# Kernel optimization log

Hardware: AMD Instinct MI355X
Metric: run time of the kernel (lower is better)

Reference implementation:

```python
import jax, jax.numpy as jnp
import numpy as np

NB_TF = 4          # brightness, contrast, invert-blend, gain
MAGS_PER_TF = 9    # magnitudes 0.1 .. 0.9 (range(1, int(mag*10)) with mag=1)
NB_OP = NB_TF * MAGS_PER_TF


def setup_inputs() -> dict:
    key = jax.random.key(0)
    k1, k2, k3 = jax.random.split(key, 3)
    B, C, H, W = 256, 3, 224, 224
    x = jax.random.uniform(k1, (B, C, H, W), dtype=jnp.float32)
    # per-image sampled op index (Categorical over a uniform distribution)
    sample = jax.random.randint(k2, (B,), 0, NB_OP)
    # per-op Bernoulli(prob=0.5) coin: 1 -> apply the op, 0 -> identity
    apply_mask = jax.random.randint(k3, (NB_OP,), 0, 2).astype(jnp.int32)
    return {"x": x, "sample": sample, "apply_mask": apply_mask}


def _apply_ops(x, sample, apply_mask):
    # Decode op index -> (tf type, magnitude). op_list layout: for tf in TFs:
    #   for m in 1..9: (tf, prob, m/10)
    tf_idx = sample // MAGS_PER_TF                       # [B]
    mag = ((sample % MAGS_PER_TF) + 1).astype(x.dtype) / 10.0
    mag = mag[:, None, None, None]                       # [B,1,1,1]

    mean = jnp.mean(x, axis=(1, 2, 3), keepdims=True)    # per-image mean
    t_bright = jnp.clip(x + mag, 0.0, 1.0)               # brightness shift
    t_contr = jnp.clip(mean + (x - mean) * (1.0 + mag), 0.0, 1.0)
    t_inv = (1.0 - mag) * x + mag * (1.0 - x)            # blend with inverted
    t_gain = jnp.clip(x * (1.0 + mag), 0.0, 1.0)         # multiplicative gain

    stack = jnp.stack([t_bright, t_contr, t_inv, t_gain], axis=1)  # [B,4,C,H,W]
    sel = tf_idx[:, None, None, None, None]              # [B,1,1,1,1]
    transformed = jnp.take_along_axis(stack, sel, axis=1)[:, 0]    # [B,C,H,W]

    applied = (apply_mask[sample] > 0)[:, None, None, None]
    return jnp.where(applied, transformed, x)


def reference(x, sample, apply_mask):
    # N_seqTF = 1 -> single round of sample -> gather -> transform -> scatter,
    # here expressed as a fully vectorized per-image select.
    return _apply_ops(x, sample, apply_mask)
```

## Files before the change

kernel.cpp:

```cpp
#include <hip/hip_runtime.h>

#define N_IMG   256
#define HW      (224 * 224)
#define CHW     (3 * HW)
#define V4      (CHW / 4)
#define THREADS 256

#define PARTS       7
#define PART_V4     (V4 / PARTS)
#define PER_THREAD  (PART_V4 / THREADS)

#define CHUNKS  (V4 / THREADS)

#define MAGS_PER_TF 9

__device__ __forceinline__ float clip01(float v) {
    return fminf(fmaxf(v, 0.0f), 1.0f);
}

__global__ __launch_bounds__(THREADS) void mean_kernel(
        const float* __restrict__ x,
        const int* __restrict__ sample,
        const int* __restrict__ apply_mask,
        float* __restrict__ partials ) {
    const int img  = blockIdx.y;
    const int part = blockIdx.x;
    const int s    = sample[img];
    const int tf   = s / MAGS_PER_TF;
    if (tf != 1 || apply_mask[s] <= 0) return;

    const float4* xp = (const float4*)x + (size_t)img * V4 + (size_t)part * PART_V4;
    float sum = 0.0f;
#pragma unroll
    for (int k = 0; k < PER_THREAD; ++k) {
        float4 v = xp[threadIdx.x + k * THREADS];
        sum += (v.x + v.y) + (v.z + v.w);
    }
#pragma unroll
    for (int off = 32; off > 0; off >>= 1)
        sum += __shfl_down(sum, off, 64);

    __shared__ float wsum[THREADS / 64];
    if ((threadIdx.x & 63) == 0) wsum[threadIdx.x >> 6] = sum;
    __syncthreads();
    if (threadIdx.x == 0) {
        float t = (wsum[0] + wsum[1]) + (wsum[2] + wsum[3]);
        partials[img * PARTS + part] = t;
    }
}

__global__ __launch_bounds__(THREADS) void apply_kernel(
        const float* __restrict__ x,
        const int* __restrict__ sample,
        const int* __restrict__ apply_mask,
        const float* __restrict__ partials,
        float* __restrict__ out) {
    const int img   = blockIdx.y;
    const int chunk = blockIdx.x;
    const int s     = sample[img];
    const int tf    = s / MAGS_PER_TF;
    const float mag = (float)(s % MAGS_PER_TF + 1) / 10.0f;
    const bool applied = apply_mask[s] > 0;

    const size_t idx = (size_t)img * V4 + (size_t)chunk * THREADS + threadIdx.x;
    const float4* xp = (const float4*)x;
    float4*       op = (float4*)out;

    float4 v = xp[idx];
    float4 r;

    if (!applied) {
        r = v;
    } else if (tf == 0) {
        r.x = clip01(v.x + mag);
        r.y = clip01(v.y + mag);
        r.z = clip01(v.z + mag);
        r.w = clip01(v.w + mag);
    } else if (tf == 1) {
        float mean = 0.0f;
#pragma unroll
        for (int p = 0; p < PARTS; ++p) mean += partials[img * PARTS + p];
        mean /= (float)CHW;
        const float g = 1.0f + mag;
        r.x = clip01(mean + (v.x - mean) * g);
        r.y = clip01(mean + (v.y - mean) * g);
        r.z = clip01(mean + (v.z - mean) * g);
        r.w = clip01(mean + (v.w - mean) * g);
    } else if (tf == 2) {
        const float a = 1.0f - mag;
        r.x = a * v.x + mag * (1.0f - v.x);
        r.y = a * v.y + mag * (1.0f - v.y);
        r.z = a * v.z + mag * (1.0f - v.z);
        r.w = a * v.w + mag * (1.0f - v.w);
    } else {
        const float g = 1.0f + mag;
        r.x = clip01(v.x * g);
        r.y = clip01(v.y * g);
        r.z = clip01(v.z * g);
        r.w = clip01(v.w * g);
    }
    op[idx] = r;
}

extern "C" void kernel_launch(void* const* d_in, const int* in_sizes, int n_in,
                              void* d_out, int out_size, void* d_ws, size_t ws_size,
                              hipStream_t stream) {
    const float* x          = (const float*)d_in[0];
    const int*   sample     = (const int*)d_in[1];
    const int*   apply_mask = (const int*)d_in[2];
    float*       out        = (float*)d_out;
    float*       partials   = (float*)d_ws;

    dim3 mgrid(PARTS, N_IMG);
    mean_kernel<<<mgrid, THREADS, 0, stream>>>(x, sample, apply_mask, partials);

    dim3 agrid(CHUNKS, N_IMG);
    apply_kernel<<<agrid, THREADS, 0, stream>>>(x, sample, apply_mask, partials, out);
}
```

Before: 262.1 us.

## Coarsen apply kernel to 7 float4 per thread with nontemporal stores

The apply kernel drops from one float4 per thread across 147 blocks per image to 7 float4 per thread across 21 blocks per image. All loads are issued before compute, and outputs are written with nontemporal stores. The mean kernel uses the same 21-chunk split and loads its values into registers first. The aim is to cut per-block overhead, raise memory-level parallelism, and keep the output stream out of cache. The cost is fewer blocks overall and more registers per thread.

```diff
diff --git a/kernel.cpp b/kernel.cpp
--- a/kernel.cpp
+++ b/kernel.cpp
@@ -6,13 +6,13 @@
 #define V4      (CHW / 4)
 #define THREADS 256
 
-#define PARTS       7
-#define PART_V4     (V4 / PARTS)
-#define PER_THREAD  (PART_V4 / THREADS)
-
-#define CHUNKS  (V4 / THREADS)
+#define CHUNKS      21
+#define CHUNK_V4    (V4 / CHUNKS)
+#define PER_THREAD  (CHUNK_V4 / THREADS)
 
 #define MAGS_PER_TF 9
+
+typedef float fvec4 __attribute__((ext_vector_type(4)));
 
 __device__ __forceinline__ float clip01(float v) {
     return fminf(fmaxf(v, 0.0f), 1.0f);
@@ -26,16 +26,19 @@
     const int img  = blockIdx.y;
     const int part = blockIdx.x;
     const int s    = sample[img];
-    const int tf   = s / MAGS_PER_TF;
-    if (tf != 1 || apply_mask[s] <= 0) return;
+    if ((s / MAGS_PER_TF) != 1 || apply_mask[s] <= 0) return;
 
-    const float4* xp = (const float4*)x + (size_t)img * V4 + (size_t)part * PART_V4;
+    const fvec4* xp = (const fvec4*)x + (size_t)img * V4 + (size_t)part * CHUNK_V4;
+    fvec4 v[PER_THREAD];
+#pragma unroll
+    for (int k = 0; k < PER_THREAD; ++k)
+        v[k] = xp[threadIdx.x + k * THREADS];
+
     float sum = 0.0f;
 #pragma unroll
-    for (int k = 0; k < PER_THREAD; ++k) {
-        float4 v = xp[threadIdx.x + k * THREADS];
-        sum += (v.x + v.y) + (v.z + v.w);
-    }
+    for (int k = 0; k < PER_THREAD; ++k)
+        sum += (v[k].x + v[k].y) + (v[k].z + v[k].w);
+
 #pragma unroll
     for (int off = 32; off > 0; off >>= 1)
         sum += __shfl_down(sum, off, 64);
@@ -45,7 +48,7 @@
     __syncthreads();
     if (threadIdx.x == 0) {
         float t = (wsum[0] + wsum[1]) + (wsum[2] + wsum[3]);
-        partials[img * PARTS + part] = t;
+        partials[img * CHUNKS + part] = t;
     }
 }
 
@@ -62,44 +65,64 @@
     const float mag = (float)(s % MAGS_PER_TF + 1) / 10.0f;
     const bool applied = apply_mask[s] > 0;
 
-    const size_t idx = (size_t)img * V4 + (size_t)chunk * THREADS + threadIdx.x;
-    const float4* xp = (const float4*)x;
-    float4*       op = (float4*)out;
+    const size_t base = (size_t)img * V4 + (size_t)chunk * CHUNK_V4 + threadIdx.x;
+    const fvec4* xp = (const fvec4*)x + base;
+    fvec4*       op = (fvec4*)out + base;
 
-    float4 v = xp[idx];
-    float4 r;
+    fvec4 v[PER_THREAD];
+#pragma unroll
+    for (int k = 0; k < PER_THREAD; ++k)
+        v[k] = xp[k * THREADS];
+
+    fvec4 r[PER_THREAD];
 
     if (!applied) {
-        r = v;
+#pragma unroll
+        for (int k = 0; k < PER_THREAD; ++k) r[k] = v[k];
     } else if (tf == 0) {
-        r.x = clip01(v.x + mag);
-        r.y = clip01(v.y + mag);
-        r.z = clip01(v.z + mag);
-        r.w = clip01(v.w + mag);
+#pragma unroll
+        for (int k = 0; k < PER_THREAD; ++k) {
+            r[k].x = clip01(v[k].x + mag);
+            r[k].y = clip01(v[k].y + mag);
+            r[k].z = clip01(v[k].z + mag);
+            r[k].w = clip01(v[k].w + mag);
+        }
     } else if (tf == 1) {
         float mean = 0.0f;
 #pragma unroll
-        for (int p = 0; p < PARTS; ++p) mean += partials[img * PARTS + p];
+        for (int p = 0; p < CHUNKS; ++p) mean += partials[img * CHUNKS + p];
         mean /= (float)CHW;
         const float g = 1.0f + mag;
-        r.x = clip01(mean + (v.x - mean) * g);
-        r.y = clip01(mean + (v.y - mean) * g);
-        r.z = clip01(mean + (v.z - mean) * g);
-        r.w = clip01(mean + (v.w - mean) * g);
+#pragma unroll
+        for (int k = 0; k < PER_THREAD; ++k) {
+            r[k].x = clip01(mean + (v[k].x - mean) * g);
+            r[k].y = clip01(mean + (v[k].y - mean) * g);
+            r[k].z = clip01(mean + (v[k].z - mean) * g);
+            r[k].w = clip01(mean + (v[k].w - mean) * g);
+        }
     } else if (tf == 2) {
         const float a = 1.0f - mag;
-        r.x = a * v.x + mag * (1.0f - v.x);
-        r.y = a * v.y + mag * (1.0f - v.y);
-        r.z = a * v.z + mag * (1.0f - v.z);
-        r.w = a * v.w + mag * (1.0f - v.w);
+#pragma unroll
+        for (int k = 0; k < PER_THREAD; ++k) {
+            r[k].x = a * v[k].x + mag * (1.0f - v[k].x);
+            r[k].y = a * v[k].y + mag * (1.0f - v[k].y);
+            r[k].z = a * v[k].z + mag * (1.0f - v[k].z);
+            r[k].w = a * v[k].w + mag * (1.0f - v[k].w);
+        }
     } else {
         const float g = 1.0f + mag;
-        r.x = clip01(v.x * g);
-        r.y = clip01(v.y * g);
-        r.z = clip01(v.z * g);
-        r.w = clip01(v.w * g);
+#pragma unroll
+        for (int k = 0; k < PER_THREAD; ++k) {
+            r[k].x = clip01(v[k].x * g);
+            r[k].y = clip01(v[k].y * g);
+            r[k].z = clip01(v[k].z * g);
+            r[k].w = clip01(v[k].w * g);
+        }
     }
-    op[idx] = r;
+
+#pragma unroll
+    for (int k = 0; k < PER_THREAD; ++k)
+        __builtin_nontemporal_store(r[k], op + k * THREADS);
 }
 
 extern "C" void kernel_launch(void* const* d_in, const int* in_sizes, int n_in,
@@ -111,7 +134,7 @@
     float*       out        = (float*)d_out;
     float*       partials   = (float*)d_ws;
 
-    dim3 mgrid(PARTS, N_IMG);
+    dim3 mgrid(CHUNKS, N_IMG);
     mean_kernel<<<mgrid, THREADS, 0, stream>>>(x, sample, apply_mask, partials);
 
     dim3 agrid(CHUNKS, N_IMG);
```

Result: slower. 274.7 us (+4.8%).
